# Optimization experiments

Hardware: AMD Instinct MI355X
Metric: run time of the kernel (lower is better)

The kernel has to match this reference:

```python
import jax, jax.numpy as jnp
import numpy as np

D_MODEL = 1024
H = 16
D_K = D_MODEL // H
B = 2
S = 2048


def setup_inputs() -> dict:
    key = jax.random.key(0)
    ks = jax.random.split(key, 13)
    scale = 1.0 / np.sqrt(D_MODEL)
    inp = {
        "Q": jax.random.normal(ks[0], (B, S, D_MODEL), jnp.float32),
        "K": jax.random.normal(ks[1], (B, S, D_MODEL), jnp.float32),
        "V": jax.random.normal(ks[2], (B, S, D_MODEL), jnp.float32),
        "mask": jax.random.randint(ks[3], (B, 1, S, S), 0, 2, jnp.int32),
        "WQ_w": jax.random.normal(ks[4], (D_MODEL, D_MODEL), jnp.float32) * scale,
        "WQ_b": jax.random.normal(ks[5], (D_MODEL,), jnp.float32) * scale,
        "WK_w": jax.random.normal(ks[6], (D_MODEL, D_MODEL), jnp.float32) * scale,
        "WK_b": jax.random.normal(ks[7], (D_MODEL,), jnp.float32) * scale,
        "WV_w": jax.random.normal(ks[8], (D_MODEL, D_MODEL), jnp.float32) * scale,
        "WV_b": jax.random.normal(ks[9], (D_MODEL,), jnp.float32) * scale,
        "WO_w": jax.random.normal(ks[10], (D_MODEL, D_MODEL), jnp.float32) * scale,
        "WO_b": jax.random.normal(ks[11], (D_MODEL,), jnp.float32) * scale,
    }
    return inp


def _split_heads(x):
    # [B,S,D] -> [B,H,S,d_k]
    b, s, _ = x.shape
    return x.reshape(b, s, H, D_K).transpose(0, 2, 1, 3)


def reference(Q, K, V, mask, WQ_w, WQ_b, WK_w, WK_b, WV_w, WV_b, WO_w, WO_b):
    q = _split_heads(Q @ WQ_w.T + WQ_b)
    k = _split_heads(K @ WK_w.T + WK_b)
    v = _split_heads(V @ WV_w.T + WV_b)
    scores = jnp.einsum("bhqd,bhkd->bhqk", q, k) / jnp.sqrt(jnp.float32(D_K))
    # NOTE: original code fills masked positions with 1e-9 (not -inf) -- replicate faithfully
    scores = jnp.where(mask == 0, jnp.float32(1e-9), scores)
    attn = jax.nn.softmax(scores, axis=-1)
    out = jnp.einsum("bhqk,bhkd->bhqd", attn, v)  # [B,H,S,d_k]
    out = out.transpose(0, 2, 1, 3).reshape(Q.shape[0], -1, D_MODEL)
    return out @ WO_w.T + WO_b
```

## Files before the change

### kernel.cpp

```cpp
#include <hip/hip_runtime.h>
#include <stdint.h>

#define D_MODEL 1024
#define NH 16
#define DKK 64
#define SEQ 2048
#define QSCALE 0.18033688011112042f

using half8 = __attribute__((ext_vector_type(8))) _Float16;
using half4 = __attribute__((ext_vector_type(4))) _Float16;
using half2v = __attribute__((ext_vector_type(2))) _Float16;
using fp16x2 = __attribute__((ext_vector_type(2))) __fp16;
using f32x4 = __attribute__((ext_vector_type(4))) float;
using f32x16 = __attribute__((ext_vector_type(16))) float;

__device__ __forceinline__ f32x4 fz4() { f32x4 v = {0.f, 0.f, 0.f, 0.f}; return v; }

__device__ __forceinline__ void gload16(const void* g, void* l) {
    __builtin_amdgcn_global_load_lds(
        (const __attribute__((address_space(1))) unsigned int*)g,
        (__attribute__((address_space(3))) unsigned int*)l, 16, 0, 0);
}

__device__ __forceinline__ half2v pk2(float a, float b) {
    fp16x2 t = __builtin_amdgcn_cvt_pkrtz(a, b);
    return __builtin_bit_cast(half2v, t);
}

__device__ __forceinline__ half4 pk4(float a, float b, float c, float d) {
    half2v lo = pk2(a, b);
    half2v hi = pk2(c, d);
    half4 r; r.x = lo.x; r.y = lo.y; r.z = hi.x; r.w = hi.y;
    return r;
}

__device__ __forceinline__ int xswz(int bid, int n) {
    return (bid & 7) * (n >> 3) + (bid >> 3);
}

__global__ __launch_bounds__(256) void prep(const float* __restrict__ wq,
                                            const float* __restrict__ wk,
                                            const float* __restrict__ wv,
                                            const float* __restrict__ wo,
                                            const float* __restrict__ Q,
                                            const float* __restrict__ K,
                                            const float* __restrict__ V,
                                            const int* __restrict__ mask,
                                            _Float16* __restrict__ out,
                                            unsigned int* __restrict__ mbits) {
    const int bid = blockIdx.x;
    if (bid < 2048) {
        int idx = bid * 256 + threadIdx.x;
#pragma unroll
        for (int k = 0; k < 8; ++k) {
            int c = idx + k * 524288;
            const float* src;
            int off;
            if (c < 1048576) {
                int w = c >> 18;
                src = (w == 0) ? wq : (w == 1) ? wk : (w == 2) ? wv : wo;
                off = c & 0x3ffff;
            } else {
                int j = (c >> 20) - 1;
                src = (j == 0) ? Q : (j == 1) ? K : V;
                off = c & 0xfffff;
            }
            float4 v = ((const float4*)src)[off];
            ((half4*)out)[c] = pk4(v.x, v.y, v.z, v.w);
        }
    } else {
        int wid = threadIdx.x >> 6, lane = threadIdx.x & 63;
        int row = (bid - 2048) * 4 + wid;
        const int* mrow = mask + (size_t)row * SEQ;
        unsigned int* orow = mbits + (size_t)row * (SEQ / 32);
        for (int it = 0; it < SEQ / 64; ++it) {
            int v = mrow[it * 64 + lane];
            unsigned long long bal = __ballot(v != 0);
            if (lane == 0)       orow[it * 2]     = (unsigned int)(bal & 0xffffffffull);
            else if (lane == 32) orow[it * 2 + 1] = (unsigned int)(bal >> 32);
        }
    }
}

__device__ __forceinline__ void gemm_body(const _Float16* __restrict__ A,
                                          const _Float16* __restrict__ Wh,
                                          const float* __restrict__ bias,
                                          void* __restrict__ outp, int omode, float scale) {
    __shared__ __align__(16) _Float16 Asm[2][64 * 64];
    __shared__ __align__(16) _Float16 Bsm[2][128 * 64];
    const int tid = threadIdx.x;
    const int wg = xswz(blockIdx.x, 512);
    const int bm = wg >> 3, bn = wg & 7;
    const int wid = tid >> 6, lane = tid & 63;
    const int li = lane & 15, g = lane >> 4;
    const int wm = wid >> 1, wn = wid & 1;

    const int brow = wid * 32 + (lane >> 3);
    const char* bsrc = (const char*)(Wh + (size_t)(bn * 128 + brow) * D_MODEL)
                       + (((lane & 7) ^ (brow & 7)) * 16);
    const int bdst = wid * 32 * 128;
    const int arow = wid * 16 + (lane >> 3);
    const char* asrc = (const char*)(A + (size_t)(bm * 64 + arow) * D_MODEL)
                       + (((lane & 7) ^ (arow & 7)) * 16);
    const int adst = wid * 16 * 128;

    f32x4 acc[2][4];
#pragma unroll
    for (int i = 0; i < 2; ++i)
#pragma unroll
        for (int j = 0; j < 4; ++j) acc[i][j] = fz4();

    const int o0 = ((g << 4))      ^ ((li & 7) << 4);
    const int o1 = (64 + (g << 4)) ^ ((li & 7) << 4);
    const int abase = wm * 4096 + li * 128;
    const int bbase = wn * 8192 + li * 128;

    auto stage = [&](int it, int buf) {
        const char* bs = bsrc + it * 128;
        char* bd = (char*)&Bsm[buf][0] + bdst;
        gload16(bs,             bd);
        gload16(bs +  8 * 2048, bd + 1024);
        gload16(bs + 16 * 2048, bd + 2048);
        gload16(bs + 24 * 2048, bd + 3072);
        const char* as = asrc + it * 128;
        char* ad = (char*)&Asm[buf][0] + adst;
        gload16(as,            ad);
        gload16(as + 8 * 2048, ad + 1024);
    };

    stage(0, 0);
    __syncthreads();

    for (int it = 0; it < 16; ++it) {
        const int cur = it & 1;
        if (it + 1 < 16) stage(it + 1, cur ^ 1);
        const char* ab = (const char*)&Asm[cur][0];
        const char* bb = (const char*)&Bsm[cur][0];
#pragma unroll
        for (int s = 0; s < 2; ++s) {
            const int oS = s ? o1 : o0;
            half8 af0 = *(const half8*)(ab + abase + 0    + oS);
            half8 af1 = *(const half8*)(ab + abase + 2048 + oS);
            half8 bf[4];
#pragma unroll
            for (int nt = 0; nt < 4; ++nt)
                bf[nt] = *(const half8*)(bb + bbase + nt * 2048 + oS);
#pragma unroll
            for (int nt = 0; nt < 4; ++nt) {
                acc[0][nt] = __builtin_amdgcn_mfma_f32_16x16x32_f16(af0, bf[nt], acc[0][nt], 0, 0, 0);
                acc[1][nt] = __builtin_amdgcn_mfma_f32_16x16x32_f16(af1, bf[nt], acc[1][nt], 0, 0, 0);
            }
        }
        __syncthreads();
    }

#pragma unroll
    for (int nt = 0; nt < 4; ++nt) {
        int n = bn * 128 + wn * 64 + nt * 16 + li;
        float bv = bias[n];
#pragma unroll
        for (int mt = 0; mt < 2; ++mt) {
            if (omode == 1) {
                int s0 = bm * 64 + wm * 32 + mt * 16 + g * 4;
                int b = (bm * 64) >> 11;
                int h = n >> 6, d = n & 63;
                half4 hv = pk4(acc[mt][nt][0] + bv, acc[mt][nt][1] + bv,
                               acc[mt][nt][2] + bv, acc[mt][nt][3] + bv);
                *(half4*)((_Float16*)outp +
                          ((((size_t)(b * NH + h)) * DKK + d) * SEQ + (s0 & (SEQ - 1)))) = hv;
            } else {
#pragma unroll
                for (int r = 0; r < 4; ++r) {
                    int m = bm * 64 + wm * 32 + mt * 16 + g * 4 + r;
                    float val = (acc[mt][nt][r] + bv) * scale;
                    if (omode == 2) {
                        ((float*)outp)[(size_t)m * D_MODEL + n] = val;
                    } else {
                        int b = m >> 11, s = m & (SEQ - 1);
                        int h = n >> 6, d = n & 63;
                        ((_Float16*)outp)[(((size_t)(b * NH + h)) * SEQ + s) * DKK + d] =
                            (_Float16)val;
                    }
                }
            }
        }
    }
}

struct QkvArgs {
    const float *b0, *b1, *b2;
    _Float16 *o0, *o1, *o2;
};

__global__ __launch_bounds__(256) void gemm_qkv(const _Float16* __restrict__ Ah,
                                                const _Float16* __restrict__ cw,
                                                QkvArgs ga) {
    const int z = blockIdx.y;
    const _Float16* A  = Ah + (size_t)z * (D_MODEL * 4096);
    const float* bi = (z == 0) ? ga.b0 : (z == 1) ? ga.b1 : ga.b2;
    _Float16*    o  = (z == 0) ? ga.o0 : (z == 1) ? ga.o1 : ga.o2;
    gemm_body(A, cw + (size_t)z * D_MODEL * D_MODEL, bi, o,
              (z == 2) ? 1 : 0, (z == 0) ? QSCALE : 1.0f);
}

__global__ __launch_bounds__(256) void gemm_out(const _Float16* __restrict__ A,
                                                const _Float16* __restrict__ cw,
                                                const float* __restrict__ bias,
                                                float* __restrict__ out) {
    gemm_body(A, cw, bias, out, 2, 1.0f);
}

__global__ __launch_bounds__(256, 4) void attn_fwd(const _Float16* __restrict__ q,
                                                   const _Float16* __restrict__ kk,
                                                   const _Float16* __restrict__ vt,
                                                   const unsigned int* __restrict__ mb,
                                                   _Float16* __restrict__ aout) {
    __shared__ __align__(16) char smem[32768];
    const int wg = xswz(blockIdx.x, 512);
    const int qblk = wg & 15, bh = wg >> 4;
    const int b = bh >> 4, h = bh & 15;
    const int tid = threadIdx.x, wid = tid >> 6, lane = tid & 63;
    const int l31 = lane & 31, hi = lane >> 5;
    const _Float16* qp = q  + (size_t)bh * SEQ * DKK;
    const _Float16* kp = kk + (size_t)bh * SEQ * DKK;
    const _Float16* vp = vt + (size_t)bh * DKK * SEQ;
    const int qrow = qblk * 128 + wid * 32 + l31;

    half8 qf[4];
#pragma unroll
    for (int s = 0; s < 4; ++s)
        qf[s] = *(const half8*)(qp + (size_t)qrow * DKK + s * 16 + hi * 8);

    half8 ones;
#pragma unroll
    for (int j = 0; j < 8; ++j) ones[j] = (_Float16)1.0f;

    const int srow = wid * 16 + (lane >> 3);
    const int sswz = ((lane & 7) ^ (srow & 7)) * 16;
    const char* ksrc = (const char*)(kp + (size_t)srow * DKK) + sswz;
    const char* vsrc = (const char*)(vp + (size_t)srow * SEQ) + sswz;
    const int sdst = wid * 2048;

    auto stage = [&](int it, int buf) {
        const char* ks = ksrc + (size_t)it * 8192;
        const char* vs = vsrc + (size_t)it * 128;
        char* kd = smem + buf * 8192 + sdst;
        char* vd = smem + 16384 + buf * 8192 + sdst;
        gload16(ks,                       kd);
        gload16(ks + 8 * 128,             kd + 1024);
        gload16(vs,                       vd);
        gload16(vs + 8 * (size_t)SEQ * 2, vd + 1024);
    };

    f32x16 O0, O1, Ol;
#pragma unroll
    for (int j = 0; j < 16; ++j) { O0[j] = 0.f; O1[j] = 0.f; Ol[j] = 0.f; }

    const unsigned int* mrow = mb + (size_t)(b * SEQ + qrow) * (SEQ / 32);

    const int v0row = l31;
    const int v1row = 32 + l31;

    stage(0, 0);
    __syncthreads();

    for (int it = 0; it < SEQ / 64; ++it) {
        const int cur = it & 1;
        if (it + 1 < SEQ / 64) stage(it + 1, cur ^ 1);
        const char* kb_ = smem + cur * 8192;
        const char* vb_ = smem + 16384 + cur * 8192;

#pragma unroll
        for (int kg = 0; kg < 2; ++kg) {
            const unsigned mw = mrow[it * 2 + kg] >> (hi * 4);
            const int krow = kg * 32 + l31;
            const int kbase = krow * 128;
            const int krx = (krow & 7);

            f32x16 st;
#pragma unroll
            for (int j = 0; j < 16; ++j) st[j] = 0.f;
            __builtin_amdgcn_s_setprio(1);
#pragma unroll
            for (int s = 0; s < 4; ++s) {
                const int c = s * 2 + hi;
                half8 kf = *(const half8*)(kb_ + kbase + ((c ^ krx) << 4));
                st = __builtin_amdgcn_mfma_f32_32x32x16_f16(kf, qf[s], st, 0, 0, 0);
            }
            __builtin_amdgcn_s_setprio(0);

            unsigned w[8];
#pragma unroll
            for (int rq = 0; rq < 4; ++rq) {
                float e0 = __builtin_amdgcn_exp2f(st[rq * 4 + 0]);
                float e1 = __builtin_amdgcn_exp2f(st[rq * 4 + 1]);
                float e2 = __builtin_amdgcn_exp2f(st[rq * 4 + 2]);
                float e3 = __builtin_amdgcn_exp2f(st[rq * 4 + 3]);
                float p0 = ((mw >> (8 * rq + 0)) & 1u) ? e0 : 1.0f;
                float p1 = ((mw >> (8 * rq + 1)) & 1u) ? e1 : 1.0f;
                float p2 = ((mw >> (8 * rq + 2)) & 1u) ? e2 : 1.0f;
                float p3 = ((mw >> (8 * rq + 3)) & 1u) ? e3 : 1.0f;
                w[2 * rq]     = __builtin_bit_cast(unsigned, pk2(p0, p1));
                w[2 * rq + 1] = __builtin_bit_cast(unsigned, pk2(p2, p3));
            }

            half8 pfrag[2];
#pragma unroll
            for (int s2 = 0; s2 < 2; ++s2) {
                unsigned a0 = w[s2 * 4 + 0], a1 = w[s2 * 4 + 1];
                unsigned a2 = w[s2 * 4 + 2], a3 = w[s2 * 4 + 3];
                unsigned t0 = (unsigned)__shfl_xor((int)(hi ? a0 : a2), 32);
                unsigned t1 = (unsigned)__shfl_xor((int)(hi ? a1 : a3), 32);
                uint4 f;
                f.x = hi ? t0 : a0;
                f.y = hi ? t1 : a1;
                f.z = hi ? a2 : t0;
                f.w = hi ? a3 : t1;
                pfrag[s2] = __builtin_bit_cast(half8, f);
            }

            __builtin_amdgcn_s_setprio(1);
#pragma unroll
            for (int s2 = 0; s2 < 2; ++s2) {
                const int c = kg * 4 + s2 * 2 + hi;
                half8 vf0 = *(const half8*)(vb_ + v0row * 128 + ((c ^ (v0row & 7)) << 4));
                half8 vf1 = *(const half8*)(vb_ + v1row * 128 + ((c ^ (v1row & 7)) << 4));
                Ol = __builtin_amdgcn_mfma_f32_32x32x16_f16(ones, pfrag[s2], Ol, 0, 0, 0);
                O0 = __builtin_amdgcn_mfma_f32_32x32x16_f16(vf0, pfrag[s2], O0, 0, 0, 0);
                O1 = __builtin_amdgcn_mfma_f32_32x32x16_f16(vf1, pfrag[s2], O1, 0, 0, 0);
            }
            __builtin_amdgcn_s_setprio(0);
        }
        __syncthreads();
    }

    float inv = 1.0f / Ol[0];
    _Float16* orow = aout + ((size_t)(b * SEQ + qrow)) * D_MODEL + h * DKK + hi * 4;
#pragma unroll
    for (int rq = 0; rq < 4; ++rq) {
        *(half4*)(orow + 8 * rq) =
            pk4(O0[rq * 4 + 0] * inv, O0[rq * 4 + 1] * inv,
                O0[rq * 4 + 2] * inv, O0[rq * 4 + 3] * inv);
        *(half4*)(orow + 32 + 8 * rq) =
            pk4(O1[rq * 4 + 0] * inv, O1[rq * 4 + 1] * inv,
                O1[rq * 4 + 2] * inv, O1[rq * 4 + 3] * inv);
    }
}

extern "C" void kernel_launch(void* const* d_in, const int* in_sizes, int n_in,
                              void* d_out, int out_size, void* d_ws, size_t ws_size,
                              hipStream_t stream) {
    const float* Q    = (const float*)d_in[0];
    const float* Kin  = (const float*)d_in[1];
    const float* Vin  = (const float*)d_in[2];
    const int*   mask = (const int*)d_in[3];
    const float* WQw = (const float*)d_in[4];
    const float* WQb = (const float*)d_in[5];
    const float* WKw = (const float*)d_in[6];
    const float* WKb = (const float*)d_in[7];
    const float* WVw = (const float*)d_in[8];
    const float* WVb = (const float*)d_in[9];
    const float* WOw = (const float*)d_in[10];
    const float* WOb = (const float*)d_in[11];

    char* w = (char*)d_ws;
    const size_t MB = 1ull << 20;
    _Float16* cw  = (_Float16*)(w);
    _Float16* Ah  = (_Float16*)(w + 8 * MB);
    _Float16* ab  = (_Float16*)(w + 8 * MB);
    _Float16* qb  = (_Float16*)(w + 32 * MB);
    _Float16* kbf = (_Float16*)(w + 40 * MB);
    _Float16* vtb = (_Float16*)(w + 48 * MB);
    unsigned int* mbits = (unsigned int*)(w + 56 * MB);

    prep<<<dim3(3072), dim3(256), 0, stream>>>(WQw, WKw, WVw, WOw, Q, Kin, Vin, mask,
                                               cw, mbits);

    QkvArgs ga;
    ga.b0 = WQb; ga.b1 = WKb; ga.b2 = WVb;
    ga.o0 = qb;  ga.o1 = kbf; ga.o2 = vtb;
    gemm_qkv<<<dim3(512, 3), dim3(256), 0, stream>>>(Ah, cw, ga);

    attn_fwd<<<dim3(512), dim3(256), 0, stream>>>(qb, kbf, vtb, mbits, ab);

    gemm_out<<<dim3(512), dim3(256), 0, stream>>>(ab, cw + 3ull * D_MODEL * D_MODEL, WOb,
                                                  (float*)d_out);
}
```

Baseline: 141.2 us.

## Software-pipeline attention so QK softmax of tile t overlaps PV of tile t-1

```diff
diff --git a/kernel.cpp b/kernel.cpp
--- a/kernel.cpp
+++ b/kernel.cpp
@@ -215,7 +215,7 @@
                                                    const _Float16* __restrict__ vt,
                                                    const unsigned int* __restrict__ mb,
                                                    _Float16* __restrict__ aout) {
-    __shared__ __align__(16) char smem[32768];
+    __shared__ __align__(16) char smem[40960];
     const int wg = xswz(blockIdx.x, 512);
     const int qblk = wg & 15, bh = wg >> 4;
     const int b = bh >> 4, h = bh & 15;
@@ -241,13 +241,15 @@
     const char* vsrc = (const char*)(vp + (size_t)srow * SEQ) + sswz;
     const int sdst = wid * 2048;
 
-    auto stage = [&](int it, int buf) {
+    auto stageK = [&](int it) {
         const char* ks = ksrc + (size_t)it * 8192;
+        char* kd = smem + (it & 1) * 8192 + sdst;
+        gload16(ks,           kd);
+        gload16(ks + 8 * 128, kd + 1024);
+    };
+    auto stageV = [&](int it) {
         const char* vs = vsrc + (size_t)it * 128;
-        char* kd = smem + buf * 8192 + sdst;
-        char* vd = smem + 16384 + buf * 8192 + sdst;
-        gload16(ks,                       kd);
-        gload16(ks + 8 * 128,             kd + 1024);
+        char* vd = smem + 16384 + (it % 3) * 8192 + sdst;
         gload16(vs,                       vd);
         gload16(vs + 8 * (size_t)SEQ * 2, vd + 1024);
     };
@@ -257,19 +259,13 @@
     for (int j = 0; j < 16; ++j) { O0[j] = 0.f; O1[j] = 0.f; Ol[j] = 0.f; }
 
     const unsigned int* mrow = mb + (size_t)(b * SEQ + qrow) * (SEQ / 32);
-
     const int v0row = l31;
     const int v1row = 32 + l31;
 
-    stage(0, 0);
-    __syncthreads();
-
-    for (int it = 0; it < SEQ / 64; ++it) {
-        const int cur = it & 1;
-        if (it + 1 < SEQ / 64) stage(it + 1, cur ^ 1);
-        const char* kb_ = smem + cur * 8192;
-        const char* vb_ = smem + 16384 + cur * 8192;
-
+    half8 pfA[2][2], pfB[2][2];
+
+    auto qksm = [&](int it, half8 (&pf)[2][2]) {
+        const char* kb_ = smem + (it & 1) * 8192;
 #pragma unroll
         for (int kg = 0; kg < 2; ++kg) {
             const unsigned mw = mrow[it * 2 + kg] >> (hi * 4);
@@ -303,8 +299,6 @@
                 w[2 * rq]     = __builtin_bit_cast(unsigned, pk2(p0, p1));
                 w[2 * rq + 1] = __builtin_bit_cast(unsigned, pk2(p2, p3));
             }
-
-            half8 pfrag[2];
 #pragma unroll
             for (int s2 = 0; s2 < 2; ++s2) {
                 unsigned a0 = w[s2 * 4 + 0], a1 = w[s2 * 4 + 1];
@@ -316,23 +310,49 @@
                 f.y = hi ? t1 : a1;
                 f.z = hi ? a2 : t0;
                 f.w = hi ? a3 : t1;
-                pfrag[s2] = __builtin_bit_cast(half8, f);
-            }
-
-            __builtin_amdgcn_s_setprio(1);
+                pf[kg][s2] = __builtin_bit_cast(half8, f);
+            }
+        }
+    };
+
+    auto pv = [&](int it, half8 (&pf)[2][2]) {
+        const char* vb_ = smem + 16384 + (it % 3) * 8192;
+        __builtin_amdgcn_s_setprio(1);
+#pragma unroll
+        for (int kg = 0; kg < 2; ++kg)
 #pragma unroll
             for (int s2 = 0; s2 < 2; ++s2) {
                 const int c = kg * 4 + s2 * 2 + hi;
                 half8 vf0 = *(const half8*)(vb_ + v0row * 128 + ((c ^ (v0row & 7)) << 4));
                 half8 vf1 = *(const half8*)(vb_ + v1row * 128 + ((c ^ (v1row & 7)) << 4));
-                Ol = __builtin_amdgcn_mfma_f32_32x32x16_f16(ones, pfrag[s2], Ol, 0, 0, 0);
-                O0 = __builtin_amdgcn_mfma_f32_32x32x16_f16(vf0, pfrag[s2], O0, 0, 0, 0);
-                O1 = __builtin_amdgcn_mfma_f32_32x32x16_f16(vf1, pfrag[s2], O1, 0, 0, 0);
-            }
-            __builtin_amdgcn_s_setprio(0);
-        }
+                Ol = __builtin_amdgcn_mfma_f32_32x32x16_f16(ones, pf[kg][s2], Ol, 0, 0, 0);
+                O0 = __builtin_amdgcn_mfma_f32_32x32x16_f16(vf0,  pf[kg][s2], O0, 0, 0, 0);
+                O1 = __builtin_amdgcn_mfma_f32_32x32x16_f16(vf1,  pf[kg][s2], O1, 0, 0, 0);
+            }
+        __builtin_amdgcn_s_setprio(0);
+    };
+
+    stageK(0); stageV(0);
+    __syncthreads();
+    stageK(1); stageV(1);
+    qksm(0, pfA);
+    __syncthreads();
+
+    for (int i2 = 0; i2 < 15; ++i2) {
+        const int t = 1 + 2 * i2;
+        stageK(t + 1); stageV(t + 1);
+        qksm(t, pfB);
+        pv(t - 1, pfA);
+        __syncthreads();
+        const int u = t + 1;
+        if (u + 1 < SEQ / 64) { stageK(u + 1); stageV(u + 1); }
+        qksm(u, pfA);
+        pv(u - 1, pfB);
         __syncthreads();
     }
+    qksm(31, pfB);
+    pv(30, pfA);
+    pv(31, pfB);
 
     float inv = 1.0f / Ol[0];
     _Float16* orow = aout + ((size_t)(b * SEQ + qrow)) * D_MODEL + h * DKK + hi * 4;
```

New measurement: 157.9 us. 11.8% more time.
